# Optimization experiments

Measured on AMD Instinct MI355X. Metric: run time of the kernel, lower is better.

Reference implementation:

```python
import jax, jax.numpy as jnp
import numpy as np

SEQ_LEN = 8
NUM_HEADS = 8
LN_EPS = 1e-5
GN_EPS = 64e-5  # GroupNorm eps = head_dim * 1e-5 (RWKV7 convention, head_dim=64)


def layer_norm(x, w, b):
    mu = x.mean(-1, keepdims=True)
    var = ((x - mu) ** 2).mean(-1, keepdims=True)
    return (x - mu) / jnp.sqrt(var + LN_EPS) * w + b


def token_shift(x):
    # delta = shift(x) - x; shift prepends one zero token along time
    return jnp.pad(x, ((0, 0), (1, 0), (0, 0)))[:, :-1] - x


def group_norm(x, w, b, H):
    B, T, C = x.shape
    xh = x.reshape(B, T, H, C // H)
    mu = xh.mean(-1, keepdims=True)
    var = ((xh - mu) ** 2).mean(-1, keepdims=True)
    return ((xh - mu) / jnp.sqrt(var + GN_EPS)).reshape(B, T, C) * w + b


def rwkv7_scan(r, w, k, v, a, b, H):
    # Generalized delta-rule recurrence (RWKV7):
    #   S_t = S_{t-1} * diag(exp(-exp(w_t))) + (S_{t-1} a_t) b_t^T + v_t k_t^T
    #   o_t = S_t r_t
    B, T, C = r.shape
    N = C // H

    def tm(x):  # [B,T,C] -> [T,B,H,N] (time-major for scan)
        return x.reshape(B, T, H, N).transpose(1, 0, 2, 3)

    decay = jnp.exp(-jnp.exp(tm(w)))
    rs, ks, vs, as_, bs = tm(r), tm(k), tm(v), tm(a), tm(b)

    def step(S, inp):
        rt, dt, kt, vt, at, bt = inp  # each [B,H,N]
        sa = jnp.einsum('bhij,bhj->bhi', S, at)
        S = (S * dt[:, :, None, :]
             + sa[..., None] * bt[:, :, None, :]
             + vt[..., None] * kt[:, :, None, :])
        return S, jnp.einsum('bhij,bhj->bhi', S, rt)

    S0 = jnp.zeros((B, H, N, N), r.dtype)
    _, out = jax.lax.scan(step, S0, (rs, decay, ks, vs, as_, bs))
    return out.transpose(1, 0, 2, 3).reshape(B, T, C)


def _forward(image_tensor, pos_emb, xm, w0, w1, w2, a0, a1, a2, v0, v1, v2,
             g1, g2, kkp, kap, rkp, Wr, Wk, Wv, Wo, lnx_w, lnx_b,
             ln1_w, ln1_b, ln2_w, ln2_b, fxk, Wkey, Wval, lnf_w, lnf_b):
    EB, C, ih, iw = image_tensor.shape
    B = EB // SEQ_LEN
    H = NUM_HEADS
    x = image_tensor.transpose(0, 2, 3, 1).reshape(EB, ih * iw, C)
    x = (x + pos_emb).reshape(B, SEQ_LEN * ih * iw, C)  # [B, T, C]
    L = Wr.shape[0]
    v_first = None
    for l in range(L):
        # ---- time mix (RWKV7 attention) ----
        h = layer_norm(x, ln1_w[l], ln1_b[l])
        Bh, T, _ = h.shape
        dx = token_shift(h)
        xr, xw, xk, xv, xa, xg = [h + dx * xm[l, i] for i in range(6)]
        r = xr @ Wr[l]
        w = -jax.nn.softplus(-(w0[l] + jnp.tanh(xw @ w1[l]) @ w2[l])) - 0.5
        k = xk @ Wk[l]
        v = xv @ Wv[l]
        if v_first is None:
            v_first = v
        else:
            v = v + (v_first - v) * jax.nn.sigmoid(v0[l] + (xv @ v1[l]) @ v2[l])
        a = jax.nn.sigmoid(a0[l] + (xa @ a1[l]) @ a2[l])  # in-context lr
        g = jax.nn.sigmoid(xg @ g1[l]) @ g2[l]
        kk = (k * kkp[l]).reshape(Bh, T, H, -1)
        kk = kk / jnp.maximum(jnp.linalg.norm(kk, axis=-1, keepdims=True), 1e-12)
        kk = kk.reshape(Bh, T, C)
        k = k * (1.0 + (a - 1.0) * kap[l])
        o = rwkv7_scan(r, w, k, v, -kk, kk * a, H)
        o = group_norm(o, lnx_w[l], lnx_b[l], H)
        r4, k4, v4 = (t.reshape(Bh, T, H, -1) for t in (r, k, v))
        o = o + ((r4 * k4 * rkp[l]).sum(-1, keepdims=True) * v4).reshape(Bh, T, C)
        x = x + (o * g) @ Wo[l]
        # ---- channel mix (squared-ReLU FFN) ----
        h = layer_norm(x, ln2_w[l], ln2_b[l])
        kf = h + token_shift(h) * fxk[l]
        x = x + jnp.square(jax.nn.relu(kf @ Wkey[l])) @ Wval[l]
    x = layer_norm(x, lnf_w, lnf_b)
    return x.reshape(EB, ih, iw, C).transpose(0, 3, 1, 2)


def setup_inputs() -> dict:
    key = jax.random.key(0)
    ks = jax.random.split(key, 24)
    L, C, H = 8, 512, 8
    DW, DA, DV, DG, FF = 64, 64, 32, 128, 2048
    EB, IV, IW = 32, 8, 16
    FS = IV * IW

    def n(k, shape, s=0.02):
        return jax.random.normal(k, shape, jnp.float32) * s

    return dict(
        image_tensor=jax.random.normal(ks[0], (EB, C, IV, IW), jnp.float32),
        pos_emb=n(ks[1], (1, FS, C)),
        xm=jax.random.uniform(ks[2], (L, 6, C), jnp.float32),
        w0=n(ks[3], (L, C), 0.5) - 0.5,
        w1=n(ks[4], (L, C, DW), 0.02), w2=n(ks[5], (L, DW, C), 0.1),
        a0=jnp.zeros((L, C), jnp.float32),
        a1=n(ks[6], (L, C, DA)), a2=n(ks[7], (L, DA, C), 0.1),
        v0=jnp.ones((L, C), jnp.float32),
        v1=n(ks[8], (L, C, DV)), v2=n(ks[9], (L, DV, C), 0.1),
        g1=n(ks[10], (L, C, DG)), g2=n(ks[11], (L, DG, C), 0.1),
        kkp=jnp.full((L, C), 0.85, jnp.float32),
        kap=jnp.ones((L, C), jnp.float32),
        rkp=n(ks[12], (L, H, C // H), 0.3),
        Wr=n(ks[13], (L, C, C)), Wk=n(ks[14], (L, C, C)),
        Wv=n(ks[15], (L, C, C)), Wo=n(ks[16], (L, C, C)),
        lnx_w=jnp.ones((L, C), jnp.float32), lnx_b=jnp.zeros((L, C), jnp.float32),
        ln1_w=jnp.ones((L, C), jnp.float32), ln1_b=jnp.zeros((L, C), jnp.float32),
        ln2_w=jnp.ones((L, C), jnp.float32), ln2_b=jnp.zeros((L, C), jnp.float32),
        fxk=jax.random.uniform(ks[17], (L, C), jnp.float32),
        Wkey=n(ks[18], (L, C, FF)), Wval=n(ks[19], (L, FF, C)),
        lnf_w=jnp.ones((C,), jnp.float32), lnf_b=jnp.zeros((C,), jnp.float32),
    )


def reference(image_tensor, pos_emb, xm, w0, w1, w2, a0, a1, a2, v0, v1, v2,
              g1, g2, kkp, kap, rkp, Wr, Wk, Wv, Wo, lnx_w, lnx_b,
              ln1_w, ln1_b, ln2_w, ln2_b, fxk, Wkey, Wval, lnf_w, lnf_b):
    return _forward(image_tensor, pos_emb, xm, w0, w1, w2, a0, a1, a2, v0, v1,
                    v2, g1, g2, kkp, kap, rkp, Wr, Wk, Wv, Wo, lnx_w, lnx_b,
                    ln1_w, ln1_b, ln2_w, ln2_b, fxk, Wkey, Wval, lnf_w, lnf_b)
```

## Files before the change

kernel.cpp:

```cpp
#include <hip/hip_runtime.h>
#include <hip/hip_bf16.h>
#include <math.h>


#define NTOK 4096
#define CDIM 512
#define TT   1024
#define LC   64
#define NCH  16
#define TB   8

#define BM 128
#define BK 32

enum { EPI_NONE=0, EPI_TANH, EPI_SIG, EPI_DECAY, EPI_SIGB, EPI_VMIX, EPI_RELU2, EPI_ADD };

typedef short bf16x8 __attribute__((ext_vector_type(8)));
typedef float f32x4 __attribute__((ext_vector_type(4)));
typedef unsigned short ushort_t;

__device__ __forceinline__ float wsum64(float v) {
#pragma unroll
  for (int s = 1; s < 64; s <<= 1) v += __shfl_xor(v, s);
  return v;
}
__device__ __forceinline__ float gsum8(float v) {
  v += __shfl_xor(v, 1); v += __shfl_xor(v, 2); v += __shfl_xor(v, 4);
  return v;
}
__device__ __forceinline__ float sigm(float z) { return 1.f / (1.f + expf(-z)); }
__device__ __forceinline__ ushort_t f2bf(float x) {
  return __builtin_bit_cast(unsigned short, __float2bfloat16(x));
}
__device__ __forceinline__ void glds16(const void* g, void* l) {
  __builtin_amdgcn_global_load_lds(
      (const __attribute__((address_space(1))) void*)g,
      (__attribute__((address_space(3))) void*)l, 16, 0, 0);
}

struct Seg {
  const ushort_t* A; const ushort_t* B; void* C;
  const float* bias; const float* e1;
  int N; int K; int epi; int obf;
};
struct Segs4 { Seg s[4]; };

template<int BNt>
__global__ __launch_bounds__(256) void ggemm_k(Segs4 segs) {
  const Seg sg = segs.s[blockIdx.z];
  if (sg.epi < 0) return;
  constexpr int NCHK = 8 + BNt / 16;
  constexpr int LPW  = NCHK / 4;
  constexpr int WNF  = BNt / 32;
  __shared__ ushort_t As[3][BM * BK];
  __shared__ ushort_t Bs[3][BNt * BK];
  const ushort_t* __restrict__ A = sg.A;
  const ushort_t* __restrict__ B = sg.B;
  const int N = sg.N, K = sg.K;
  const int tid = threadIdx.x;
  const int wave = tid >> 6, lane = tid & 63;
  const int m0 = blockIdx.x * BM, n0 = blockIdx.y * BNt;
  const int wm = (wave >> 1) << 6, wn = (wave & 1) * (BNt / 2);

  f32x4 zero = {0.f, 0.f, 0.f, 0.f};
  f32x4 acc[4][WNF];
#pragma unroll
  for (int i = 0; i < 4; ++i)
#pragma unroll
    for (int j = 0; j < WNF; ++j) acc[i][j] = zero;

  const int crow = lane >> 2;
  const int soff = (((lane & 3) ^ (crow & 3)) << 3);
  const ushort_t* gptr[LPW];
  ushort_t* lbase[LPW];
  int lstr[LPW];
#pragma unroll
  for (int i = 0; i < LPW; ++i) {
    const int c = wave + 4 * i;
    if (c < 8) {
      gptr[i] = A + (size_t)(m0 + c * 16 + crow) * K + soff;
      lbase[i] = &As[0][c * 512 + lane * 8];
      lstr[i] = BM * BK;
    } else {
      gptr[i] = B + (size_t)(n0 + (c - 8) * 16 + crow) * K + soff;
      lbase[i] = &Bs[0][(c - 8) * 512 + lane * 8];
      lstr[i] = BNt * BK;
    }
  }

#define STAGE(bf_, k0_)                                        \
  { _Pragma("unroll") for (int i = 0; i < LPW; ++i)            \
      glds16(gptr[i] + (k0_), lbase[i] + (bf_) * lstr[i]); }

  const int rA = wm + (lane & 15);
  const int rB = wn + (lane & 15);
  const int kb = (((lane >> 4) ^ (lane & 3)) << 3);

#define COMPUTE(bf_)                                                          \
  {                                                                           \
    bf16x8 av[4], bvv[WNF];                                                   \
    _Pragma("unroll") for (int f = 0; f < 4; ++f)                             \
      av[f] = *(const bf16x8*)(&As[bf_][(rA + f * 16) * 32 + kb]);            \
    _Pragma("unroll") for (int f = 0; f < WNF; ++f)                           \
      bvv[f] = *(const bf16x8*)(&Bs[bf_][(rB + f * 16) * 32 + kb]);           \
    _Pragma("unroll") for (int i = 0; i < 4; ++i)                             \
      _Pragma("unroll") for (int j = 0; j < WNF; ++j)                         \
        acc[i][j] = __builtin_amdgcn_mfma_f32_16x16x32_bf16(av[i], bvv[j],    \
                                                            acc[i][j], 0, 0, 0); \
  }

  const int nk = K / BK;
  STAGE(0, 0);
  if (nk > 1) STAGE(1, BK);
  int bc = 0, bs = 2;
  for (int k = 0; k + 1 < nk; ++k) {
    asm volatile("s_waitcnt vmcnt(%0)" :: "i"(LPW) : "memory");
    __builtin_amdgcn_s_barrier();
    if (k + 2 < nk) {
      STAGE(bs, (k + 2) * BK);
      bs = (bs == 2) ? 0 : bs + 1;
    }
    COMPUTE(bc);
    bc = (bc == 2) ? 0 : bc + 1;
  }
  asm volatile("s_waitcnt vmcnt(0)" ::: "memory");
  __builtin_amdgcn_s_barrier();
  COMPUTE(bc);
#undef STAGE
#undef COMPUTE

  void* Cout = sg.C;
  const float* bias = sg.bias;
  const float* e1 = sg.e1;
  const int em = m0 + wm + ((lane >> 4) << 2);
  const int en = n0 + wn + (lane & 15);

#define EPI_STORE(EPI_, OBF_)                                                 \
  { _Pragma("unroll") for (int fi = 0; fi < 4; ++fi) {                        \
      _Pragma("unroll") for (int fj = 0; fj < WNF; ++fj) {                    \
        const int gn = en + fj * 16;                                          \
        if (gn < N) {                                                         \
          _Pragma("unroll") for (int rr = 0; rr < 4; ++rr) {                  \
            const int gm = em + fi * 16 + rr;                                 \
            const size_t idx = (size_t)gm * N + gn;                           \
            const float y = acc[fi][fj][rr];                                  \
            float outv;                                                       \
            if (EPI_ == EPI_NONE) { outv = y; }                               \
            else if (EPI_ == EPI_TANH) { outv = tanhf(y); }                   \
            else if (EPI_ == EPI_SIG) { outv = sigm(y); }                     \
            else if (EPI_ == EPI_DECAY) {                                     \
              const float z = bias[gn] + y;                                   \
              const float w = -log1pf(expf(-z)) - 0.5f;                       \
              outv = expf(-expf(w));                                          \
            } else if (EPI_ == EPI_SIGB) { outv = sigm(bias[gn] + y); }       \
            else if (EPI_ == EPI_VMIX) {                                      \
              const float vr = ((float*)Cout)[idx];                           \
              outv = vr + (e1[idx] - vr) * sigm(bias[gn] + y);                \
            } else if (EPI_ == EPI_RELU2) {                                   \
              const float t = fmaxf(y, 0.f); outv = t * t;                    \
            } else { outv = ((float*)Cout)[idx] + y; }                        \
            if (OBF_) ((ushort_t*)Cout)[idx] = f2bf(outv);                    \
            else      ((float*)Cout)[idx] = outv;                             \
          }                                                                   \
        }                                                                     \
      } } }

  switch (sg.epi) {
    case EPI_NONE:  if (sg.obf) EPI_STORE(EPI_NONE, 1) else EPI_STORE(EPI_NONE, 0); break;
    case EPI_TANH:  EPI_STORE(EPI_TANH, 1); break;
    case EPI_SIG:   EPI_STORE(EPI_SIG, 1); break;
    case EPI_DECAY: EPI_STORE(EPI_DECAY, 0); break;
    case EPI_SIGB:  EPI_STORE(EPI_SIGB, 0); break;
    case EPI_VMIX:  EPI_STORE(EPI_VMIX, 0); break;
    case EPI_RELU2: EPI_STORE(EPI_RELU2, 1); break;
    case EPI_ADD:   EPI_STORE(EPI_ADD, 0); break;
  }
#undef EPI_STORE
}

__global__ __launch_bounds__(256) void wprep_k(
    const float* __restrict__ in, ushort_t* __restrict__ out,
    int K, int N, int Npad)
{
  __shared__ float t[32][33];
  const int l = blockIdx.z;
  const int n0 = blockIdx.x * 32, k0 = blockIdx.y * 32;
  const int tx = threadIdx.x & 31, ty = threadIdx.x >> 5;
  const float* src = in + (size_t)l * K * N;
  ushort_t* dst = out + (size_t)l * Npad * K;
#pragma unroll
  for (int i = 0; i < 32; i += 8) {
    const int k = k0 + ty + i, n = n0 + tx;
    t[ty + i][tx] = (n < N) ? src[(size_t)k * N + n] : 0.f;
  }
  __syncthreads();
#pragma unroll
  for (int i = 0; i < 32; i += 8) {
    const int n = n0 + ty + i, k = k0 + tx;
    dst[(size_t)n * K + k] = f2bf(t[tx][ty + i]);
  }
}

__global__ __launch_bounds__(256) void lnmix6_k(
    const float* __restrict__ x, const float* __restrict__ w,
    const float* __restrict__ b, const float* __restrict__ xml,
    ushort_t* __restrict__ xr, ushort_t* __restrict__ xw,
    ushort_t* __restrict__ xk, ushort_t* __restrict__ xv,
    ushort_t* __restrict__ xa, ushort_t* __restrict__ xg)
{
  const int m = blockIdx.x * 4 + (threadIdx.x >> 6);
  const int lane = threadIdx.x & 63;
  const int c0 = lane << 3;
  const size_t idx = (size_t)m * CDIM + c0;
  const bool first = ((m & (TT - 1)) == 0);
  float v[8], p[8];
  *(float4*)&v[0] = *(const float4*)&x[idx];
  *(float4*)&v[4] = *(const float4*)&x[idx + 4];
  if (first) {
#pragma unroll
    for (int j = 0; j < 8; ++j) p[j] = 0.f;
  } else {
    *(float4*)&p[0] = *(const float4*)&x[idx - CDIM];
    *(float4*)&p[4] = *(const float4*)&x[idx - CDIM + 4];
  }
  float s = 0.f, sp = 0.f;
#pragma unroll
  for (int j = 0; j < 8; ++j) { s += v[j]; sp += p[j]; }
  s = wsum64(s); sp = wsum64(sp);
  const float mu = s * (1.f / 512.f), mup = sp * (1.f / 512.f);
  float q = 0.f, qp = 0.f;
#pragma unroll
  for (int j = 0; j < 8; ++j) {
    const float d1 = v[j] - mu, d2 = p[j] - mup;
    q += d1 * d1; qp += d2 * d2;
  }
  q = wsum64(q); qp = wsum64(qp);
  const float is = rsqrtf(q * (1.f / 512.f) + 1e-5f);
  const float isp = rsqrtf(qp * (1.f / 512.f) + 1e-5f);
  float wc[8], bc[8];
  *(float4*)&wc[0] = *(const float4*)&w[c0]; *(float4*)&wc[4] = *(const float4*)&w[c0 + 4];
  *(float4*)&bc[0] = *(const float4*)&b[c0]; *(float4*)&bc[4] = *(const float4*)&b[c0 + 4];
  float hv[8], dx[8];
#pragma unroll
  for (int j = 0; j < 8; ++j) {
    hv[j] = (v[j] - mu) * is * wc[j] + bc[j];
    const float hp = first ? 0.f : (p[j] - mup) * isp * wc[j] + bc[j];
    dx[j] = hp - hv[j];
  }
  ushort_t* outs[6] = {xr, xw, xk, xv, xa, xg};
#pragma unroll
  for (int o = 0; o < 6; ++o) {
    float mc[8];
    *(float4*)&mc[0] = *(const float4*)&xml[o * CDIM + c0];
    *(float4*)&mc[4] = *(const float4*)&xml[o * CDIM + c0 + 4];
    bf16x8 pk;
#pragma unroll
    for (int j = 0; j < 8; ++j) pk[j] = (short)f2bf(fmaf(dx[j], mc[j], hv[j]));
    *(bf16x8*)&outs[o][idx] = pk;
  }
}

__global__ __launch_bounds__(256) void lnmix1_k(
    const float* __restrict__ x, const float* __restrict__ w,
    const float* __restrict__ b, const float* __restrict__ coef,
    ushort_t* __restrict__ kf)
{
  const int m = blockIdx.x * 4 + (threadIdx.x >> 6);
  const int lane = threadIdx.x & 63;
  const int c0 = lane << 3;
  const size_t idx = (size_t)m * CDIM + c0;
  const bool first = ((m & (TT - 1)) == 0);
  float v[8], p[8];
  *(float4*)&v[0] = *(const float4*)&x[idx];
  *(float4*)&v[4] = *(const float4*)&x[idx + 4];
  if (first) {
#pragma unroll
    for (int j = 0; j < 8; ++j) p[j] = 0.f;
  } else {
    *(float4*)&p[0] = *(const float4*)&x[idx - CDIM];
    *(float4*)&p[4] = *(const float4*)&x[idx - CDIM + 4];
  }
  float s = 0.f, sp = 0.f;
#pragma unroll
  for (int j = 0; j < 8; ++j) { s += v[j]; sp += p[j]; }
  s = wsum64(s); sp = wsum64(sp);
  const float mu = s * (1.f / 512.f), mup = sp * (1.f / 512.f);
  float q = 0.f, qp = 0.f;
#pragma unroll
  for (int j = 0; j < 8; ++j) {
    const float d1 = v[j] - mu, d2 = p[j] - mup;
    q += d1 * d1; qp += d2 * d2;
  }
  q = wsum64(q); qp = wsum64(qp);
  const float is = rsqrtf(q * (1.f / 512.f) + 1e-5f);
  const float isp = rsqrtf(qp * (1.f / 512.f) + 1e-5f);
  bf16x8 pk;
#pragma unroll
  for (int j = 0; j < 8; ++j) {
    const float wc = w[c0 + j], bc = b[c0 + j];
    const float hv = (v[j] - mu) * is * wc + bc;
    const float hp = first ? 0.f : (p[j] - mup) * isp * wc + bc;
    pk[j] = (short)f2bf(fmaf(hp - hv, coef[c0 + j], hv));
  }
  *(bf16x8*)&kf[idx] = pk;
}

__global__ __launch_bounds__(256) void prep_k(
    float* __restrict__ k, const float* __restrict__ a,
    const float* __restrict__ kkp, const float* __restrict__ kap,
    float* __restrict__ aa, float* __restrict__ bb)
{
  const int m = blockIdx.x * 4 + (threadIdx.x >> 6);
  const int lane = threadIdx.x & 63;
  const int c0 = lane << 3;
  const size_t idx = (size_t)m * CDIM + c0;
  float kv[8], av[8], kp[8], ka[8];
  *(float4*)&kv[0] = *(const float4*)&k[idx];     *(float4*)&kv[4] = *(const float4*)&k[idx + 4];
  *(float4*)&av[0] = *(const float4*)&a[idx];     *(float4*)&av[4] = *(const float4*)&a[idx + 4];
  *(float4*)&kp[0] = *(const float4*)&kkp[c0];    *(float4*)&kp[4] = *(const float4*)&kkp[c0 + 4];
  *(float4*)&ka[0] = *(const float4*)&kap[c0];    *(float4*)&ka[4] = *(const float4*)&kap[c0 + 4];
  float kk[8], ss = 0.f;
#pragma unroll
  for (int j = 0; j < 8; ++j) { kk[j] = kv[j] * kp[j]; ss += kk[j] * kk[j]; }
  ss = gsum8(ss);
  const float rden = 1.f / fmaxf(sqrtf(ss), 1e-12f);
  float oaa[8], obb[8], okk[8];
#pragma unroll
  for (int j = 0; j < 8; ++j) {
    const float kkn = kk[j] * rden;
    oaa[j] = -kkn;
    obb[j] = kkn * av[j];
    okk[j] = kv[j] * (1.f + (av[j] - 1.f) * ka[j]);
  }
  *(float4*)&aa[idx] = *(float4*)&oaa[0]; *(float4*)&aa[idx + 4] = *(float4*)&oaa[4];
  *(float4*)&bb[idx] = *(float4*)&obb[0]; *(float4*)&bb[idx + 4] = *(float4*)&obb[4];
  *(float4*)&k[idx]  = *(float4*)&okk[0]; *(float4*)&k[idx + 4]  = *(float4*)&okk[4];
}

__global__ __launch_bounds__(256) void post_k(
    const float* __restrict__ o, const float* __restrict__ r,
    const float* __restrict__ k, const float* __restrict__ v,
    const float* __restrict__ g, const float* __restrict__ gw,
    const float* __restrict__ gb, const float* __restrict__ rkp,
    ushort_t* __restrict__ og)
{
  const int m = blockIdx.x * 4 + (threadIdx.x >> 6);
  const int lane = threadIdx.x & 63;
  const int c0 = lane << 3;
  const size_t idx = (size_t)m * CDIM + c0;
  float ov[8], rv[8], kv[8], vv[8], gv[8], rp[8];
  *(float4*)&ov[0] = *(const float4*)&o[idx];   *(float4*)&ov[4] = *(const float4*)&o[idx + 4];
  *(float4*)&rv[0] = *(const float4*)&r[idx];   *(float4*)&rv[4] = *(const float4*)&r[idx + 4];
  *(float4*)&kv[0] = *(const float4*)&k[idx];   *(float4*)&kv[4] = *(const float4*)&k[idx + 4];
  *(float4*)&vv[0] = *(const float4*)&v[idx];   *(float4*)&vv[4] = *(const float4*)&v[idx + 4];
  *(float4*)&gv[0] = *(const float4*)&g[idx];   *(float4*)&gv[4] = *(const float4*)&g[idx + 4];
  *(float4*)&rp[0] = *(const float4*)&rkp[c0];  *(float4*)&rp[4] = *(const float4*)&rkp[c0 + 4];
  float s = 0.f, dot = 0.f;
#pragma unroll
  for (int j = 0; j < 8; ++j) { s += ov[j]; dot += rv[j] * kv[j] * rp[j]; }
  s = gsum8(s); dot = gsum8(dot);
  const float mu = s * (1.f / 64.f);
  float q = 0.f;
#pragma unroll
  for (int j = 0; j < 8; ++j) { const float d = ov[j] - mu; q += d * d; }
  q = gsum8(q);
  const float is = rsqrtf(q * (1.f / 64.f) + 64e-5f);
  bf16x8 pk;
#pragma unroll
  for (int j = 0; j < 8; ++j) {
    const float gn = (ov[j] - mu) * is * gw[c0 + j] + gb[c0 + j];
    pk[j] = (short)f2bf((gn + dot * vv[j]) * gv[j]);
  }
  *(bf16x8*)&og[idx] = pk;
}

__global__ __launch_bounds__(512) void ln_final_k(
    const float* __restrict__ x, const float* __restrict__ w,
    const float* __restrict__ b, float* __restrict__ out)
{
  const int m = blockIdx.x, c = threadIdx.x;
  const size_t idx = (size_t)m * CDIM + c;
  const float v = x[idx];
  __shared__ float red[8], red2[8];
  float s = wsum64(v);
  if ((c & 63) == 0) red[c >> 6] = s;
  __syncthreads();
  float tot = 0.f;
#pragma unroll
  for (int u = 0; u < 8; ++u) tot += red[u];
  const float mu = tot * (1.f / 512.f);
  const float dv = v - mu;
  float s2 = wsum64(dv * dv);
  if ((c & 63) == 0) red2[c >> 6] = s2;
  __syncthreads();
  float vt = 0.f;
#pragma unroll
  for (int u = 0; u < 8; ++u) vt += red2[u];
  const float y = dv * rsqrtf(vt * (1.f / 512.f) + 1e-5f) * w[c] + b[c];
  const int bidx = m >> 10, t = m & 1023;
  const int p = t & 127, eb = bidx * 8 + (t >> 7);
  out[((size_t)eb * CDIM + c) * 128 + p] = y;
}

__global__ __launch_bounds__(512) void build_x_k(
    const float* __restrict__ img, const float* __restrict__ pos,
    float* __restrict__ x)
{
  const int m = blockIdx.x, c = threadIdx.x;
  const int bidx = m >> 10, t = m & 1023;
  const int p = t & 127, eb = bidx * 8 + (t >> 7);
  x[(size_t)m * CDIM + c] =
      img[((size_t)eb * CDIM + c) * 128 + p] + pos[(size_t)p * CDIM + c];
}

__global__ __launch_bounds__(256) void scan1_k(
    const float* __restrict__ d, const float* __restrict__ k,
    const float* __restrict__ v, const float* __restrict__ aa,
    const float* __restrict__ bb,
    float* __restrict__ P, float* __restrict__ Q)
{
  const int ch = blockIdx.x, bh = blockIdx.y;
  const int b = bh >> 3, hh = bh & 7;
  const int tid = threadIdx.x;
  const int i = tid >> 2, j0 = (tid & 3) << 4;
  float S[16], Pr[16];
#pragma unroll
  for (int u = 0; u < 16; ++u) { S[u] = 0.f; Pr[u] = (j0 + u == i) ? 1.f : 0.f; }

  __shared__ float sbuf[2][5 * TB * 64];
  const size_t base = (size_t)b * TT * CDIM + (size_t)ch * LC * CDIM + hh * 64;
  const float* srcs[5] = {d, k, v, aa, bb};
  const int f0 = tid, f1 = tid + 256, f2 = tid + 512;
  const float* gp0 = srcs[f0 >> 7] + base + (size_t)((f0 >> 4) & 7) * CDIM + ((f0 & 15) << 2);
  const float* gp1 = srcs[f1 >> 7] + base + (size_t)((f1 >> 4) & 7) * CDIM + ((f1 & 15) << 2);
  const float* gp2 = (tid < 128)
      ? srcs[f2 >> 7] + base + (size_t)((f2 >> 4) & 7) * CDIM + ((f2 & 15) << 2)
      : srcs[0];

#define STAGE1(bf_, goff_)                                   \
  {                                                          \
    glds16(gp0 + (goff_), &sbuf[bf_][f0 << 2]);              \
    glds16(gp1 + (goff_), &sbuf[bf_][f1 << 2]);              \
    if (tid < 128) glds16(gp2 + (goff_), &sbuf[bf_][f2 << 2]); \
  }

  STAGE1(0, 0);
  __syncthreads();
  int buf = 0;
  for (int g = 0; g < LC / TB; ++g) {
    if (g + 1 < LC / TB) STAGE1(buf ^ 1, (size_t)(g + 1) * TB * CDIM);
    const float* sb0 = sbuf[buf];
#pragma unroll
    for (int tt = 0; tt < TB; ++tt) {
      const float* sd = sb0 + 0 * TB * 64 + tt * 64;
      const float* sk = sb0 + 1 * TB * 64 + tt * 64;
      const float* sv = sb0 + 2 * TB * 64 + tt * 64;
      const float* sa = sb0 + 3 * TB * 64 + tt * 64;
      const float* sbv = sb0 + 4 * TB * 64 + tt * 64;

      float ps = 0.f, pp = 0.f;
#pragma unroll
      for (int jj = 0; jj < 16; ++jj) {
        ps = fmaf(S[jj],  sa[j0 + jj], ps);
        pp = fmaf(Pr[jj], sa[j0 + jj], pp);
      }
      ps += __shfl_xor(ps, 1); ps += __shfl_xor(ps, 2);
      pp += __shfl_xor(pp, 1); pp += __shfl_xor(pp, 2);
      const float vi = sv[i];
#pragma unroll
      for (int jj = 0; jj < 16; ++jj) {
        S[jj]  = fmaf(S[jj],  sd[j0 + jj], fmaf(ps, sbv[j0 + jj], vi * sk[j0 + jj]));
        Pr[jj] = fmaf(Pr[jj], sd[j0 + jj], pp * sbv[j0 + jj]);
      }
    }
    __syncthreads();
    buf ^= 1;
  }
#undef STAGE1

  const size_t ob = ((size_t)(bh * NCH + ch)) * 4096 + (size_t)i * 64 + j0;
#pragma unroll
  for (int u = 0; u < 4; ++u) {
    *(float4*)&Q[ob + 4 * u] = make_float4(S[4*u], S[4*u+1], S[4*u+2], S[4*u+3]);
    *(float4*)&P[ob + 4 * u] = make_float4(Pr[4*u], Pr[4*u+1], Pr[4*u+2], Pr[4*u+3]);
  }
}

__global__ __launch_bounds__(512) void scan2_k(
    const float* __restrict__ P, const float* __restrict__ Q,
    float* __restrict__ Sst)
{
  const int tid = threadIdx.x;
  const int f0 = tid << 2;
  const int r0 = tid >> 4;
  const int c0 = (tid & 15) << 2;
  __shared__ float sP[4096];
  __shared__ float sS[4096];
  float4 S0 = {0.f, 0.f, 0.f, 0.f}, S1 = {0.f, 0.f, 0.f, 0.f};
  const size_t cbase = (size_t)blockIdx.x * NCH * 4096;
  float4 pf0 = *(const float4*)&P[cbase + f0];
  float4 pf1 = *(const float4*)&P[cbase + f0 + 2048];

  for (int c = 0; c < NCH; ++c) {
    const size_t cb = cbase + (size_t)c * 4096;
    *(float4*)&Sst[cb + f0] = S0;
    *(float4*)&Sst[cb + f0 + 2048] = S1;
    __syncthreads();
    *(float4*)&sP[f0] = pf0;  *(float4*)&sP[f0 + 2048] = pf1;
    *(float4*)&sS[f0] = S0;   *(float4*)&sS[f0 + 2048] = S1;
    __syncthreads();
    if (c + 1 < NCH) {
      pf0 = *(const float4*)&P[cb + 4096 + f0];
      pf1 = *(const float4*)&P[cb + 4096 + f0 + 2048];
    }
    const float4 q0 = *(const float4*)&Q[cb + f0];
    const float4 q1 = *(const float4*)&Q[cb + f0 + 2048];

    float a00 = 0.f, a01 = 0.f, a02 = 0.f, a03 = 0.f;
    float a10 = 0.f, a11 = 0.f, a12 = 0.f, a13 = 0.f;
    const float* sS0 = &sS[r0 * 64];
    const float* sS1 = &sS[(r0 + 32) * 64];
#pragma unroll
    for (int mm = 0; mm < 64; ++mm) {
      const float4 p4 = *(const float4*)&sP[mm * 64 + c0];
      const float u0 = sS0[mm], u1 = sS1[mm];
      a00 = fmaf(u0, p4.x, a00); a01 = fmaf(u0, p4.y, a01);
      a02 = fmaf(u0, p4.z, a02); a03 = fmaf(u0, p4.w, a03);
      a10 = fmaf(u1, p4.x, a10); a11 = fmaf(u1, p4.y, a11);
      a12 = fmaf(u1, p4.z, a12); a13 = fmaf(u1, p4.w, a13);
    }
    S0.x = a00 + q0.x; S0.y = a01 + q0.y; S0.z = a02 + q0.z; S0.w = a03 + q0.w;
    S1.x = a10 + q1.x; S1.y = a11 + q1.y; S1.z = a12 + q1.z; S1.w = a13 + q1.w;
  }
}

__global__ __launch_bounds__(256) void scan3_k(
    const float* __restrict__ r, const float* __restrict__ d,
    const float* __restrict__ k, const float* __restrict__ v,
    const float* __restrict__ aa, const float* __restrict__ bb,
    const float* __restrict__ Sst, float* __restrict__ o)
{
  const int ch = blockIdx.x, bh = blockIdx.y;
  const int b = bh >> 3, hh = bh & 7;
  const int tid = threadIdx.x;
  const int i = tid >> 2, q = tid & 3, j0 = q << 4;
  float S[16];
  const size_t sb_ = ((size_t)(bh * NCH + ch)) * 4096 + (size_t)i * 64 + j0;
#pragma unroll
  for (int u = 0; u < 4; ++u) {
    const float4 s4 = *(const float4*)&Sst[sb_ + 4 * u];
    S[4*u] = s4.x; S[4*u+1] = s4.y; S[4*u+2] = s4.z; S[4*u+3] = s4.w;
  }

  __shared__ float sbuf[2][6 * TB * 64];
  const size_t base = (size_t)b * TT * CDIM + (size_t)ch * LC * CDIM + hh * 64;
  const float* srcs[6] = {r, d, k, v, aa, bb};
  const int f0 = tid, f1 = tid + 256, f2 = tid + 512;
  const float* gp0 = srcs[f0 >> 7] + base + (size_t)((f0 >> 4) & 7) * CDIM + ((f0 & 15) << 2);
  const float* gp1 = srcs[f1 >> 7] + base + (size_t)((f1 >> 4) & 7) * CDIM + ((f1 & 15) << 2);
  const float* gp2 = srcs[f2 >> 7] + base + (size_t)((f2 >> 4) & 7) * CDIM + ((f2 & 15) << 2);

#define STAGE3(bf_, goff_)                          \
  {                                                 \
    glds16(gp0 + (goff_), &sbuf[bf_][f0 << 2]);     \
    glds16(gp1 + (goff_), &sbuf[bf_][f1 << 2]);     \
    glds16(gp2 + (goff_), &sbuf[bf_][f2 << 2]);     \
  }

  STAGE3(0, 0);
  __syncthreads();
  int buf = 0;
  for (int g = 0; g < LC / TB; ++g) {
    if (g + 1 < LC / TB) STAGE3(buf ^ 1, (size_t)(g + 1) * TB * CDIM);
    const float* sb0 = sbuf[buf];
    const size_t obase = base + (size_t)g * TB * CDIM;
#pragma unroll
    for (int tt = 0; tt < TB; ++tt) {
      const float* sr = sb0 + 0 * TB * 64 + tt * 64;
      const float* sd = sb0 + 1 * TB * 64 + tt * 64;
      const float* sk = sb0 + 2 * TB * 64 + tt * 64;
      const float* sv = sb0 + 3 * TB * 64 + tt * 64;
      const float* sa = sb0 + 4 * TB * 64 + tt * 64;
      const float* sbv = sb0 + 5 * TB * 64 + tt * 64;

      float ps = 0.f, ps1 = 0.f;
#pragma unroll
      for (int jj = 0; jj < 16; jj += 2) {
        ps  = fmaf(S[jj],     sa[j0 + jj],     ps);
        ps1 = fmaf(S[jj + 1], sa[j0 + jj + 1], ps1);
      }
      ps += ps1;
      ps += __shfl_xor(ps, 1); ps += __shfl_xor(ps, 2);
      const float vi = sv[i];

      float po = 0.f, po1 = 0.f;
#pragma unroll
      for (int jj = 0; jj < 16; jj += 2) {
        float s0 = fmaf(S[jj],     sd[j0 + jj],     fmaf(ps, sbv[j0 + jj],     vi * sk[j0 + jj]));
        float s1 = fmaf(S[jj + 1], sd[j0 + jj + 1], fmaf(ps, sbv[j0 + jj + 1], vi * sk[j0 + jj + 1]));
        S[jj] = s0; S[jj + 1] = s1;
        po  = fmaf(s0, sr[j0 + jj],     po);
        po1 = fmaf(s1, sr[j0 + jj + 1], po1);
      }
      po += po1;
      po += __shfl_xor(po, 1); po += __shfl_xor(po, 2);
      if (q == 0) o[obase + (size_t)tt * CDIM + i] = po;
    }
    __syncthreads();
    buf ^= 1;
  }
#undef STAGE3
}

extern "C" void kernel_launch(void* const* d_in, const int* in_sizes, int n_in,
                              void* d_out, int out_size, void* d_ws, size_t ws_size,
                              hipStream_t stream) {
  (void)in_sizes; (void)n_in; (void)out_size; (void)ws_size;
  const float* img  = (const float*)d_in[0];
  const float* pos  = (const float*)d_in[1];
  const float* xm   = (const float*)d_in[2];
  const float* w0   = (const float*)d_in[3];
  const float* w1   = (const float*)d_in[4];
  const float* w2   = (const float*)d_in[5];
  const float* a0   = (const float*)d_in[6];
  const float* a1   = (const float*)d_in[7];
  const float* a2   = (const float*)d_in[8];
  const float* v0   = (const float*)d_in[9];
  const float* v1   = (const float*)d_in[10];
  const float* v2   = (const float*)d_in[11];
  const float* g1   = (const float*)d_in[12];
  const float* g2   = (const float*)d_in[13];
  const float* kkp  = (const float*)d_in[14];
  const float* kap  = (const float*)d_in[15];
  const float* rkp  = (const float*)d_in[16];
  const float* Wr   = (const float*)d_in[17];
  const float* Wk   = (const float*)d_in[18];
  const float* Wv   = (const float*)d_in[19];
  const float* Wo   = (const float*)d_in[20];
  const float* lnxw = (const float*)d_in[21];
  const float* lnxb = (const float*)d_in[22];
  const float* ln1w = (const float*)d_in[23];
  const float* ln1b = (const float*)d_in[24];
  const float* ln2w = (const float*)d_in[25];
  const float* ln2b = (const float*)d_in[26];
  const float* fxk  = (const float*)d_in[27];
  const float* Wkey = (const float*)d_in[28];
  const float* Wval = (const float*)d_in[29];
  const float* lnfw = (const float*)d_in[30];
  const float* lnfb = (const float*)d_in[31];

  float* ws = (float*)d_ws;
  const size_t SZ = (size_t)NTOK * CDIM;
  float* x   = ws + 0 * SZ;
  float* r_  = ws + 2 * SZ;
  float* dec = ws + 3 * SZ;
  float* k_  = ws + 4 * SZ;
  float* v_  = ws + 5 * SZ;
  float* vf  = ws + 6 * SZ;
  float* a_  = ws + 7 * SZ;
  float* g_  = ws + 8 * SZ;
  float* aa  = ws + 9 * SZ;
  float* bb  = ws + 10 * SZ;
  float* o_  = ws + 11 * SZ;
  float* mixf = ws + 12 * SZ;
  ushort_t* xr = (ushort_t*)mixf;
  ushort_t* xw = xr + SZ;
  ushort_t* xk = xr + 2 * SZ;
  ushort_t* xv = xr + 3 * SZ;
  ushort_t* xa = xr + 4 * SZ;
  ushort_t* xg = xr + 5 * SZ;
  float* Pbuf = mixf;
  float* Qbuf = mixf + SZ;
  float* Sst  = mixf + 2 * SZ;
  ushort_t* tmpb = (ushort_t*)(ws + 15 * SZ);
  ushort_t* t0b = tmpb;
  ushort_t* t1b = tmpb + (size_t)NTOK * 64;
  ushort_t* t2b = tmpb + (size_t)NTOK * 128;
  ushort_t* t3b = tmpb + (size_t)NTOK * 160;
  ushort_t* tfb  = (ushort_t*)(ws + 15 * SZ + SZ / 2);
  ushort_t* ogb  = (ushort_t*)(ws + 17 * SZ + SZ / 2);
  ushort_t* wb   = (ushort_t*)(ws + 18 * SZ);

  const size_t oWr  = 0;
  const size_t oWk  = oWr  + (size_t)8 * 512 * 512;
  const size_t oWv  = oWk  + (size_t)8 * 512 * 512;
  const size_t oWo  = oWv  + (size_t)8 * 512 * 512;
  const size_t oW1  = oWo  + (size_t)8 * 512 * 512;
  const size_t oW2  = oW1  + (size_t)8 * 128 * 512;
  const size_t oA1  = oW2  + (size_t)8 * 512 * 64;
  const size_t oA2  = oA1  + (size_t)8 * 128 * 512;
  const size_t oV1  = oA2  + (size_t)8 * 512 * 64;
  const size_t oV2  = oV1  + (size_t)8 * 128 * 512;
  const size_t oG1  = oV2  + (size_t)8 * 512 * 32;
  const size_t oG2  = oG1  + (size_t)8 * 128 * 512;
  const size_t oKey = oG2  + (size_t)8 * 512 * 128;
  const size_t oVal = oKey + (size_t)8 * 2048 * 512;

#define WPREP(src, dst, K_, N_, NP_) \
  wprep_k<<<dim3((NP_) / 32, (K_) / 32, 8), 256, 0, stream>>>(src, dst, K_, N_, NP_)
  WPREP(Wr,   wb + oWr,  512, 512, 512);
  WPREP(Wk,   wb + oWk,  512, 512, 512);
  WPREP(Wv,   wb + oWv,  512, 512, 512);
  WPREP(Wo,   wb + oWo,  512, 512, 512);
  WPREP(w1,   wb + oW1,  512, 64,  128);
  WPREP(w2,   wb + oW2,  64,  512, 512);
  WPREP(a1,   wb + oA1,  512, 64,  128);
  WPREP(a2,   wb + oA2,  64,  512, 512);
  WPREP(v1,   wb + oV1,  512, 32,  128);
  WPREP(v2,   wb + oV2,  32,  512, 512);
  WPREP(g1,   wb + oG1,  512, 128, 128);
  WPREP(g2,   wb + oG2,  128, 512, 512);
  WPREP(Wkey, wb + oKey, 512, 2048, 2048);
  WPREP(Wval, wb + oVal, 2048, 512, 512);
#undef WPREP

  build_x_k<<<NTOK, 512, 0, stream>>>(img, pos, x);

  for (int l = 0; l < 8; ++l) {
    const size_t lc = (size_t)l * CDIM;
    const float* xml = xm + (size_t)l * 6 * CDIM;
    const ushort_t* bWr = wb + oWr + (size_t)l * 512 * 512;
    const ushort_t* bWk = wb + oWk + (size_t)l * 512 * 512;
    const ushort_t* bWv = wb + oWv + (size_t)l * 512 * 512;
    const ushort_t* bWo = wb + oWo + (size_t)l * 512 * 512;
    const ushort_t* bW1 = wb + oW1 + (size_t)l * 128 * 512;
    const ushort_t* bW2 = wb + oW2 + (size_t)l * 512 * 64;
    const ushort_t* bA1 = wb + oA1 + (size_t)l * 128 * 512;
    const ushort_t* bA2 = wb + oA2 + (size_t)l * 512 * 64;
    const ushort_t* bV1 = wb + oV1 + (size_t)l * 128 * 512;
    const ushort_t* bV2 = wb + oV2 + (size_t)l * 512 * 32;
    const ushort_t* bG1 = wb + oG1 + (size_t)l * 128 * 512;
    const ushort_t* bG2 = wb + oG2 + (size_t)l * 512 * 128;
    const ushort_t* bKy = wb + oKey + (size_t)l * 2048 * 512;
    const ushort_t* bVl = wb + oVal + (size_t)l * 512 * 2048;
    float* vdst = (l == 0) ? vf : v_;

    lnmix6_k<<<NTOK / 4, 256, 0, stream>>>(x, ln1w + lc, ln1b + lc, xml,
                                           xr, xw, xk, xv, xa, xg);
    Segs4 qkv;
    qkv.s[0] = {xr, bWr, r_,   0, 0, 512, 512, EPI_NONE, 0};
    qkv.s[1] = {xk, bWk, k_,   0, 0, 512, 512, EPI_NONE, 0};
    qkv.s[2] = {xv, bWv, vdst, 0, 0, 512, 512, EPI_NONE, 0};
    qkv.s[3] = {0, 0, 0, 0, 0, 0, 0, -1, 0};
    ggemm_k<64><<<dim3(NTOK / BM, 8, 3), 256, 0, stream>>>(qkv);

    Segs4 dn;
    dn.s[0] = {xw, bW1, t0b, 0, 0, 64,  512, EPI_TANH, 1};
    dn.s[1] = {xa, bA1, t1b, 0, 0, 64,  512, EPI_NONE, 1};
    dn.s[2] = {xv, bV1, t2b, 0, 0, 32,  512, EPI_NONE, 1};
    dn.s[3] = {xg, bG1, t3b, 0, 0, 128, 512, EPI_SIG,  1};
    ggemm_k<64><<<dim3(NTOK / BM, 2, 4), 256, 0, stream>>>(dn);

    Segs4 up;
    up.s[0] = {t0b, bW2, dec, w0 + lc, 0,  512, 64,  EPI_DECAY, 0};
    up.s[1] = {t1b, bA2, a_,  a0 + lc, 0,  512, 64,  EPI_SIGB,  0};
    up.s[2] = {t2b, bV2, v_,  v0 + lc, vf, 512, 32,  (l > 0) ? EPI_VMIX : -1, 0};
    up.s[3] = {t3b, bG2, g_,  0, 0,        512, 128, EPI_NONE,  0};
    ggemm_k<64><<<dim3(NTOK / BM, 8, 4), 256, 0, stream>>>(up);

    const float* vptr = (l == 0) ? vf : v_;
    prep_k<<<NTOK / 4, 256, 0, stream>>>(k_, a_, kkp + lc, kap + lc, aa, bb);
    scan1_k<<<dim3(NCH, 32), 256, 0, stream>>>(dec, k_, vptr, aa, bb, Pbuf, Qbuf);
    scan2_k<<<32, 512, 0, stream>>>(Pbuf, Qbuf, Sst);
    scan3_k<<<dim3(NCH, 32), 256, 0, stream>>>(r_, dec, k_, vptr, aa, bb, Sst, o_);
    post_k<<<NTOK / 4, 256, 0, stream>>>(o_, r_, k_, vptr, g_, lnxw + lc, lnxb + lc,
                                         rkp + lc, ogb);
    Segs4 wo;
    wo.s[0] = {ogb, bWo, x, 0, 0, 512, 512, EPI_ADD, 0};
    wo.s[1] = wo.s[2] = wo.s[3] = {0, 0, 0, 0, 0, 0, 0, -1, 0};
    ggemm_k<64><<<dim3(NTOK / BM, 8, 1), 256, 0, stream>>>(wo);

    lnmix1_k<<<NTOK / 4, 256, 0, stream>>>(x, ln2w + lc, ln2b + lc, fxk + lc, xr);
    Segs4 f1;
    f1.s[0] = {xr, bKy, tfb, 0, 0, 2048, 512, EPI_RELU2, 1};
    f1.s[1] = f1.s[2] = f1.s[3] = {0, 0, 0, 0, 0, 0, 0, -1, 0};
    ggemm_k<64><<<dim3(NTOK / BM, 32, 1), 256, 0, stream>>>(f1);
    Segs4 f2;
    f2.s[0] = {tfb, bVl, x, 0, 0, 512, 2048, EPI_ADD, 0};
    f2.s[1] = f2.s[2] = f2.s[3] = {0, 0, 0, 0, 0, 0, 0, -1, 0};
    ggemm_k<64><<<dim3(NTOK / BM, 8, 1), 256, 0, stream>>>(f2);
  }

  ln_final_k<<<NTOK, 512, 0, stream>>>(x, lnfw, lnfb, (float*)d_out);
}
```

Before: 2.248 ms.

## Triple-buffer scan chunk loads with explicit vmcnt waits and a single barrier

The scan1 and scan3 kernels move from double to triple buffering of the per-group LDS staging area. Loads are issued two groups ahead, and each group needs only one barrier, guarded by an explicit s_waitcnt vmcnt, instead of a full __syncthreads before and after compute. The aim is to hide global-to-LDS load latency behind the sequential recurrence and cut barrier stalls. It costs more LDS per block, which can lower occupancy. The hand-set vmcnt counts also depend on how outstanding memory operations are counted, and the output stores issued in scan3 may interfere with that count.

Result: no change. 2.250 ms (+0.1%).

```diff
diff --git a/kernel.cpp b/kernel.cpp
--- a/kernel.cpp
+++ b/kernel.cpp
@@ -427,7 +427,7 @@
 #pragma unroll
   for (int u = 0; u < 16; ++u) { S[u] = 0.f; Pr[u] = (j0 + u == i) ? 1.f : 0.f; }
 
-  __shared__ float sbuf[2][5 * TB * 64];
+  __shared__ float sbuf[3][5 * TB * 64];
   const size_t base = (size_t)b * TT * CDIM + (size_t)ch * LC * CDIM + hh * 64;
   const float* srcs[5] = {d, k, v, aa, bb};
   const int f0 = tid, f1 = tid + 256, f2 = tid + 512;
@@ -437,46 +437,57 @@
       ? srcs[f2 >> 7] + base + (size_t)((f2 >> 4) & 7) * CDIM + ((f2 & 15) << 2)
       : srcs[0];
 
-#define STAGE1(bf_, goff_)                                   \
-  {                                                          \
-    glds16(gp0 + (goff_), &sbuf[bf_][f0 << 2]);              \
-    glds16(gp1 + (goff_), &sbuf[bf_][f1 << 2]);              \
+#define STAGE1(bf_, goff_)                                     \
+  {                                                            \
+    glds16(gp0 + (goff_), &sbuf[bf_][f0 << 2]);                \
+    glds16(gp1 + (goff_), &sbuf[bf_][f1 << 2]);                \
     if (tid < 128) glds16(gp2 + (goff_), &sbuf[bf_][f2 << 2]); \
   }
 
+#define CGRP1(bf_)                                                              \
+  {                                                                             \
+    const float* sb0 = sbuf[bf_];                                               \
+    _Pragma("unroll") for (int tt = 0; tt < TB; ++tt) {                         \
+      const float* sd  = sb0 + 0 * TB * 64 + tt * 64;                           \
+      const float* sk  = sb0 + 1 * TB * 64 + tt * 64;                           \
+      const float* sv  = sb0 + 2 * TB * 64 + tt * 64;                           \
+      const float* sa  = sb0 + 3 * TB * 64 + tt * 64;                           \
+      const float* sbv = sb0 + 4 * TB * 64 + tt * 64;                           \
+      float ps = 0.f, pp = 0.f;                                                 \
+      _Pragma("unroll") for (int jj = 0; jj < 16; ++jj) {                       \
+        ps = fmaf(S[jj],  sa[j0 + jj], ps);                                     \
+        pp = fmaf(Pr[jj], sa[j0 + jj], pp);                                     \
+      }                                                                         \
+      ps += __shfl_xor(ps, 1); ps += __shfl_xor(ps, 2);                         \
+      pp += __shfl_xor(pp, 1); pp += __shfl_xor(pp, 2);                         \
+      const float vi = sv[i];                                                   \
+      _Pragma("unroll") for (int jj = 0; jj < 16; ++jj) {                       \
+        S[jj]  = fmaf(S[jj],  sd[j0 + jj], fmaf(ps, sbv[j0 + jj], vi * sk[j0 + jj])); \
+        Pr[jj] = fmaf(Pr[jj], sd[j0 + jj], pp * sbv[j0 + jj]);                  \
+      }                                                                         \
+    }                                                                           \
+  }
+
+  constexpr int NG = LC / TB;
   STAGE1(0, 0);
-  __syncthreads();
-  int buf = 0;
-  for (int g = 0; g < LC / TB; ++g) {
-    if (g + 1 < LC / TB) STAGE1(buf ^ 1, (size_t)(g + 1) * TB * CDIM);
-    const float* sb0 = sbuf[buf];
-#pragma unroll
-    for (int tt = 0; tt < TB; ++tt) {
-      const float* sd = sb0 + 0 * TB * 64 + tt * 64;
-      const float* sk = sb0 + 1 * TB * 64 + tt * 64;
-      const float* sv = sb0 + 2 * TB * 64 + tt * 64;
-      const float* sa = sb0 + 3 * TB * 64 + tt * 64;
-      const float* sbv = sb0 + 4 * TB * 64 + tt * 64;
-
-      float ps = 0.f, pp = 0.f;
-#pragma unroll
-      for (int jj = 0; jj < 16; ++jj) {
-        ps = fmaf(S[jj],  sa[j0 + jj], ps);
-        pp = fmaf(Pr[jj], sa[j0 + jj], pp);
-      }
-      ps += __shfl_xor(ps, 1); ps += __shfl_xor(ps, 2);
-      pp += __shfl_xor(pp, 1); pp += __shfl_xor(pp, 2);
-      const float vi = sv[i];
-#pragma unroll
-      for (int jj = 0; jj < 16; ++jj) {
-        S[jj]  = fmaf(S[jj],  sd[j0 + jj], fmaf(ps, sbv[j0 + jj], vi * sk[j0 + jj]));
-        Pr[jj] = fmaf(Pr[jj], sd[j0 + jj], pp * sbv[j0 + jj]);
-      }
+  STAGE1(1, (size_t)TB * CDIM);
+  int bc = 0, bs = 2;
+  for (int g = 0; g + 1 < NG; ++g) {
+    if (tid < 128) { asm volatile("s_waitcnt vmcnt(3)" ::: "memory"); }
+    else           { asm volatile("s_waitcnt vmcnt(2)" ::: "memory"); }
+    __builtin_amdgcn_s_barrier();
+    if (g + 2 < NG) {
+      STAGE1(bs, (size_t)(g + 2) * TB * CDIM);
+      bs = (bs == 2) ? 0 : bs + 1;
     }
-    __syncthreads();
-    buf ^= 1;
-  }
+    CGRP1(bc);
+    bc = (bc == 2) ? 0 : bc + 1;
+  }
+  asm volatile("s_waitcnt vmcnt(0)" ::: "memory");
+  __builtin_amdgcn_s_barrier();
+  CGRP1(bc);
 #undef STAGE1
+#undef CGRP1
 
   const size_t ob = ((size_t)(bh * NCH + ch)) * 4096 + (size_t)i * 64 + j0;
 #pragma unroll
@@ -552,7 +563,7 @@
     S[4*u] = s4.x; S[4*u+1] = s4.y; S[4*u+2] = s4.z; S[4*u+3] = s4.w;
   }
 
-  __shared__ float sbuf[2][6 * TB * 64];
+  __shared__ float sbuf[3][6 * TB * 64];
   const size_t base = (size_t)b * TT * CDIM + (size_t)ch * LC * CDIM + hh * 64;
   const float* srcs[6] = {r, d, k, v, aa, bb};
   const int f0 = tid, f1 = tid + 256, f2 = tid + 512;
@@ -567,49 +578,58 @@
     glds16(gp2 + (goff_), &sbuf[bf_][f2 << 2]);     \
   }
 
+#define CGRP3(bf_, g_)                                                          \
+  {                                                                             \
+    const float* sb0 = sbuf[bf_];                                               \
+    const size_t obase = base + (size_t)(g_) * TB * CDIM;                       \
+    _Pragma("unroll") for (int tt = 0; tt < TB; ++tt) {                         \
+      const float* sr  = sb0 + 0 * TB * 64 + tt * 64;                           \
+      const float* sd  = sb0 + 1 * TB * 64 + tt * 64;                           \
+      const float* sk  = sb0 + 2 * TB * 64 + tt * 64;                           \
+      const float* sv  = sb0 + 3 * TB * 64 + tt * 64;                           \
+      const float* sa  = sb0 + 4 * TB * 64 + tt * 64;                           \
+      const float* sbv = sb0 + 5 * TB * 64 + tt * 64;                           \
+      float ps = 0.f, ps1 = 0.f;                                                \
+      _Pragma("unroll") for (int jj = 0; jj < 16; jj += 2) {                    \
+        ps  = fmaf(S[jj],     sa[j0 + jj],     ps);                             \
+        ps1 = fmaf(S[jj + 1], sa[j0 + jj + 1], ps1);                            \
+      }                                                                         \
+      ps += ps1;                                                                \
+      ps += __shfl_xor(ps, 1); ps += __shfl_xor(ps, 2);                         \
+      const float vi = sv[i];                                                   \
+      float po = 0.f, po1 = 0.f;                                                \
+      _Pragma("unroll") for (int jj = 0; jj < 16; jj += 2) {                    \
+        float s0 = fmaf(S[jj],     sd[j0 + jj],     fmaf(ps, sbv[j0 + jj],     vi * sk[j0 + jj])); \
+        float s1 = fmaf(S[jj + 1], sd[j0 + jj + 1], fmaf(ps, sbv[j0 + jj + 1], vi * sk[j0 + jj + 1])); \
+        S[jj] = s0; S[jj + 1] = s1;                                             \
+        po  = fmaf(s0, sr[j0 + jj],     po);                                    \
+        po1 = fmaf(s1, sr[j0 + jj + 1], po1);                                   \
+      }                                                                         \
+      po += po1;                                                                \
+      po += __shfl_xor(po, 1); po += __shfl_xor(po, 2);                         \
+      if (q == 0) o[obase + (size_t)tt * CDIM + i] = po;                        \
+    }                                                                           \
+  }
+
+  constexpr int NG = LC / TB;
   STAGE3(0, 0);
-  __syncthreads();
-  int buf = 0;
-  for (int g = 0; g < LC / TB; ++g) {
-    if (g + 1 < LC / TB) STAGE3(buf ^ 1, (size_t)(g + 1) * TB * CDIM);
-    const float* sb0 = sbuf[buf];
-    const size_t obase = base + (size_t)g * TB * CDIM;
-#pragma unroll
-    for (int tt = 0; tt < TB; ++tt) {
-      const float* sr = sb0 + 0 * TB * 64 + tt * 64;
-      const float* sd = sb0 + 1 * TB * 64 + tt * 64;
-      const float* sk = sb0 + 2 * TB * 64 + tt * 64;
-      const float* sv = sb0 + 3 * TB * 64 + tt * 64;
-      const float* sa = sb0 + 4 * TB * 64 + tt * 64;
-      const float* sbv = sb0 + 5 * TB * 64 + tt * 64;
-
-      float ps = 0.f, ps1 = 0.f;
-#pragma unroll
-      for (int jj = 0; jj < 16; jj += 2) {
-        ps  = fmaf(S[jj],     sa[j0 + jj],     ps);
-        ps1 = fmaf(S[jj + 1], sa[j0 + jj + 1], ps1);
-      }
-      ps += ps1;
-      ps += __shfl_xor(ps, 1); ps += __shfl_xor(ps, 2);
-      const float vi = sv[i];
-
-      float po = 0.f, po1 = 0.f;
-#pragma unroll
-      for (int jj = 0; jj < 16; jj += 2) {
-        float s0 = fmaf(S[jj],     sd[j0 + jj],     fmaf(ps, sbv[j0 + jj],     vi * sk[j0 + jj]));
-        float s1 = fmaf(S[jj + 1], sd[j0 + jj + 1], fmaf(ps, sbv[j0 + jj + 1], vi * sk[j0 + jj + 1]));
-        S[jj] = s0; S[jj + 1] = s1;
-        po  = fmaf(s0, sr[j0 + jj],     po);
-        po1 = fmaf(s1, sr[j0 + jj + 1], po1);
-      }
-      po += po1;
-      po += __shfl_xor(po, 1); po += __shfl_xor(po, 2);
-      if (q == 0) o[obase + (size_t)tt * CDIM + i] = po;
+  STAGE3(1, (size_t)TB * CDIM);
+  int bc = 0, bs = 2;
+  for (int g = 0; g + 1 < NG; ++g) {
+    asm volatile("s_waitcnt vmcnt(3)" ::: "memory");
+    __builtin_amdgcn_s_barrier();
+    if (g + 2 < NG) {
+      STAGE3(bs, (size_t)(g + 2) * TB * CDIM);
+      bs = (bs == 2) ? 0 : bs + 1;
     }
-    __syncthreads();
-    buf ^= 1;
-  }
+    CGRP3(bc, g);
+    bc = (bc == 2) ? 0 : bc + 1;
+  }
+  asm volatile("s_waitcnt vmcnt(0)" ::: "memory");
+  __builtin_amdgcn_s_barrier();
+  CGRP3(bc, NG - 1);
 #undef STAGE3
+#undef CGRP3
 }
 
 extern "C" void kernel_launch(void* const* d_in, const int* in_sizes, int n_in,
```
